# Kernel optimization log

Measured on AMD Instinct MI355X. Metric: run time of the kernel, lower is better.

## Reference

```python
import jax, jax.numpy as jnp
import numpy as np

VIS_DIM, TXT_DIM, HID = 2048, 1024, 1024


def setup_inputs() -> dict:
    key = jax.random.key(0)
    ks = jax.random.split(key, 8)
    def lin(kw, kb, fan_in, fan_out):
        bound = 1.0 / np.sqrt(fan_in)
        W = jax.random.uniform(kw, (fan_out, fan_in), jnp.float32, -bound, bound)
        b = jax.random.uniform(kb, (fan_out,), jnp.float32, -bound, bound)
        return W, b
    Wv, bv = lin(ks[0], ks[1], VIS_DIM, HID)
    Wt, bt = lin(ks[2], ks[3], TXT_DIM, HID)
    Wa, ba = lin(ks[4], ks[5], HID, 1)
    return {
        "visual_features": jax.random.normal(ks[6], (128, 256, VIS_DIM), jnp.float32),
        "text_features": jax.random.normal(ks[7], (128, TXT_DIM), jnp.float32),
        "Wv": Wv, "bv": bv, "Wt": Wt, "bt": bt, "Wa": Wa, "ba": ba,
    }


def reference(visual_features, text_features, Wv, bv, Wt, bt, Wa, ba):
    # v: (B, R, H); t: (B, 1, H) broadcast over regions
    v = jnp.einsum("brd,hd->brh", visual_features, Wv) + bv
    t = (text_features @ Wt.T + bt)[:, None, :]
    combined = jnp.tanh(v + t)                       # (B, R, H)
    scores = jnp.einsum("brh,h->br", combined, Wa[0]) + ba[0]  # (B, R)
    attention_weights = jax.nn.softmax(scores, axis=1)
    attended = jnp.einsum("br,brd->bd", attention_weights, visual_features)
    return attended, attention_weights
```

## Files before the change

kernel.cpp:

```cpp
#include <hip/hip_runtime.h>
#include <hip/hip_bf16.h>

#define VIS_DIM 2048
#define TXT_DIM 1024
#define HID     1024
#define NB      128
#define NR      256
#define M_TOT   (NB*NR)

typedef __attribute__((ext_vector_type(4))) float  f32x4;
typedef __attribute__((ext_vector_type(8))) short  short8;
typedef __attribute__((ext_vector_type(4))) unsigned short u16x4;

static __device__ __forceinline__ unsigned short f2bf(float f) {
    union { __hip_bfloat16 h; unsigned short u; } c;
    c.h = __float2bfloat16(f);
    return c.u;
}

static __device__ __forceinline__ float tanh_fast(float x) {
    float xc = fminf(fmaxf(x, -15.f), 15.f);
    float e  = __expf(2.f * xc);
    return (e - 1.f) / (e + 1.f);
}

__global__ void init_ws(float* __restrict__ scores, float* __restrict__ tbuf,
                        const float* __restrict__ bt) {
    int i = blockIdx.x * 256 + threadIdx.x;
    if (i < M_TOT) scores[i] = 0.f;
    tbuf[i] = bt[i & (HID - 1)];
}

__global__ __launch_bounds__(256) void gemm_text(const float* __restrict__ text,
                                                 const float* __restrict__ Wt,
                                                 float* __restrict__ tbuf) {
    __shared__ float As[128][33];
    __shared__ float Bs[32][33];
    const int n0  = blockIdx.x * 32;
    const int k0  = blockIdx.y * 256;
    const int tid = threadIdx.x;
    const int tm  = tid >> 3;
    const int tn  = tid & 7;
    float acc[4][4] = {};
    for (int kt = 0; kt < 8; ++kt) {
        const int k = k0 + kt * 32;
        {
            int row = tid >> 1, off = (tid & 1) * 16;
            const float* src = text + row * TXT_DIM + k + off;
            #pragma unroll
            for (int j = 0; j < 4; ++j) {
                f32x4 v = *(const f32x4*)(src + j * 4);
                As[row][off + j*4 + 0] = v.x; As[row][off + j*4 + 1] = v.y;
                As[row][off + j*4 + 2] = v.z; As[row][off + j*4 + 3] = v.w;
            }
        }
        {
            int row = tid >> 3, off = (tid & 7) * 4;
            f32x4 v = *(const f32x4*)(Wt + (size_t)(n0 + row) * TXT_DIM + k + off);
            Bs[row][off + 0] = v.x; Bs[row][off + 1] = v.y;
            Bs[row][off + 2] = v.z; Bs[row][off + 3] = v.w;
        }
        __syncthreads();
        #pragma unroll
        for (int kk = 0; kk < 32; ++kk) {
            float a[4], b[4];
            #pragma unroll
            for (int i = 0; i < 4; ++i) a[i] = As[tm*4 + i][kk];
            #pragma unroll
            for (int j = 0; j < 4; ++j) b[j] = Bs[tn*4 + j][kk];
            #pragma unroll
            for (int i = 0; i < 4; ++i)
                #pragma unroll
                for (int j = 0; j < 4; ++j) acc[i][j] += a[i] * b[j];
        }
        __syncthreads();
    }
    #pragma unroll
    for (int i = 0; i < 4; ++i)
        #pragma unroll
        for (int j = 0; j < 4; ++j)
            atomicAdd(&tbuf[(tm*4 + i) * HID + n0 + tn*4 + j], acc[i][j]);
}

#define BK 32
#define NT (VIS_DIM / BK)

static __device__ __forceinline__ int tile_off(int row, int kElem) {
    return row * 64 + (((kElem >> 3) ^ ((row >> 1) & 3)) << 4);
}

__global__ __launch_bounds__(256, 2) void gemm_vis(
        const float* __restrict__ A,
        const float* __restrict__ Bv,
        const float* __restrict__ bv,
        const float* __restrict__ wa,
        const float* __restrict__ tbuf,
        float* __restrict__ scores) {
    __shared__ __align__(16) char lds[32768];

    const int wg   = blockIdx.x;
    const int xcd  = wg & 7;
    const int loc  = wg >> 3;
    const int mb   = xcd * 32 + (loc >> 3);
    const int nb   = loc & 7;
    const int brow = mb * 128;
    const int bcol = nb * 128;

    const int tid  = threadIdx.x;
    const int lane = tid & 63;
    const int wid  = tid >> 6;
    const int wr   = wid >> 1, wc = wid & 1;

    const int srow = tid >> 3;
    const int sfs  = tid & 7;
    unsigned va0 = ((unsigned)(brow + srow      ) * VIS_DIM + sfs * 4) * 4u;
    unsigned va1 = va0 + 32u * VIS_DIM * 4u;
    unsigned va2 = va0 + 64u * VIS_DIM * 4u;
    unsigned va3 = va0 + 96u * VIS_DIM * 4u;
    unsigned vb0 = ((unsigned)(bcol + srow      ) * VIS_DIM + sfs * 4) * 4u;
    unsigned vb1 = vb0 + 32u * VIS_DIM * 4u;
    unsigned vb2 = vb0 + 64u * VIS_DIM * 4u;
    unsigned vb3 = vb0 + 96u * VIS_DIM * 4u;

    int wbyte[4];
    #pragma unroll
    for (int r = 0; r < 4; ++r) {
        int row = srow + 32 * r;
        wbyte[r] = row * 64 + (((sfs >> 1) ^ ((row >> 1) & 3)) << 4) + (sfs & 1) * 8;
    }

    f32x4 sA0, sA1, sA2, sA3, sB0, sB1, sB2, sB3;
    f32x4 tA0, tA1, tA2, tA3, tB0, tB1, tB2, tB3;
    f32x4 acc[4][4] = {};

#define GLOAD_SET(dA0,dA1,dA2,dA3,dB0,dB1,dB2,dB3)                             \
    do {                                                                       \
        asm volatile("global_load_dwordx4 %0, %1, %2"                          \
                     : "=&v"(dA0) : "v"(va0), "s"(A) : "memory");              \
        asm volatile("global_load_dwordx4 %0, %1, %2"                          \
                     : "=&v"(dA1) : "v"(va1), "s"(A) : "memory");              \
        asm volatile("global_load_dwordx4 %0, %1, %2"                          \
                     : "=&v"(dA2) : "v"(va2), "s"(A) : "memory");              \
        asm volatile("global_load_dwordx4 %0, %1, %2"                          \
                     : "=&v"(dA3) : "v"(va3), "s"(A) : "memory");              \
        asm volatile("global_load_dwordx4 %0, %1, %2"                          \
                     : "=&v"(dB0) : "v"(vb0), "s"(Bv) : "memory");             \
        asm volatile("global_load_dwordx4 %0, %1, %2"                          \
                     : "=&v"(dB1) : "v"(vb1), "s"(Bv) : "memory");             \
        asm volatile("global_load_dwordx4 %0, %1, %2"                          \
                     : "=&v"(dB2) : "v"(vb2), "s"(Bv) : "memory");             \
        asm volatile("global_load_dwordx4 %0, %1, %2"                          \
                     : "=&v"(dB3) : "v"(vb3), "s"(Bv) : "memory");             \
        va0 += BK * 4; va1 += BK * 4; va2 += BK * 4; va3 += BK * 4;            \
        vb0 += BK * 4; vb1 += BK * 4; vb2 += BK * 4; vb3 += BK * 4;            \
    } while (0)

#define GLOAD_S() GLOAD_SET(sA0,sA1,sA2,sA3,sB0,sB1,sB2,sB3)
#define GLOAD_T() GLOAD_SET(tA0,tA1,tA2,tA3,tB0,tB1,tB2,tB3)

#define VWAIT(N)                                                               \
    do {                                                                       \
        __builtin_amdgcn_sched_barrier(0);                                     \
        asm volatile("s_waitcnt vmcnt(" #N ")" ::: "memory");                  \
        __builtin_amdgcn_sched_barrier(0);                                     \
    } while (0)

#define CVT8(dst, v0)                                                          \
    do {                                                                       \
        u16x4 t_;                                                              \
        t_.x = f2bf((v0).x); t_.y = f2bf((v0).y);                              \
        t_.z = f2bf((v0).z); t_.w = f2bf((v0).w);                              \
        dst = t_;                                                              \
    } while (0)

#define LWRITE_SET(bufbase, dA0,dA1,dA2,dA3,dB0,dB1,dB2,dB3)                   \
    do {                                                                       \
        u16x4 w_;                                                              \
        char* la = lds + (bufbase);                                            \
        char* lb = lds + (bufbase) + 8192;                                     \
        CVT8(w_, dA0); *(u16x4*)(la + wbyte[0]) = w_;                          \
        CVT8(w_, dA1); *(u16x4*)(la + wbyte[1]) = w_;                          \
        CVT8(w_, dA2); *(u16x4*)(la + wbyte[2]) = w_;                          \
        CVT8(w_, dA3); *(u16x4*)(la + wbyte[3]) = w_;                          \
        CVT8(w_, dB0); *(u16x4*)(lb + wbyte[0]) = w_;                          \
        CVT8(w_, dB1); *(u16x4*)(lb + wbyte[1]) = w_;                          \
        CVT8(w_, dB2); *(u16x4*)(lb + wbyte[2]) = w_;                          \
        CVT8(w_, dB3); *(u16x4*)(lb + wbyte[3]) = w_;                          \
    } while (0)

#define LWRITE_S(bufbase) LWRITE_SET(bufbase, sA0,sA1,sA2,sA3,sB0,sB1,sB2,sB3)
#define LWRITE_T(bufbase) LWRITE_SET(bufbase, tA0,tA1,tA2,tA3,tB0,tB1,tB2,tB3)

#define COMPUTE(bufbase)                                                       \
    do {                                                                       \
        short8 af[4], bf[4];                                                   \
        const int kk = (lane >> 4) * 8;                                        \
        const char* la = lds + (bufbase);                                      \
        const char* lb = lds + (bufbase) + 8192;                               \
        _Pragma("unroll")                                                      \
        for (int m = 0; m < 4; ++m)                                            \
            af[m] = *(const short8*)(la + tile_off(wr*64 + m*16 + (lane&15), kk)); \
        _Pragma("unroll")                                                      \
        for (int n = 0; n < 4; ++n)                                            \
            bf[n] = *(const short8*)(lb + tile_off(wc*64 + n*16 + (lane&15), kk)); \
        _Pragma("unroll")                                                      \
        for (int m = 0; m < 4; ++m)                                            \
            _Pragma("unroll")                                                  \
            for (int n = 0; n < 4; ++n)                                        \
                acc[m][n] = __builtin_amdgcn_mfma_f32_16x16x32_bf16(           \
                    af[m], bf[n], acc[m][n], 0, 0, 0);                         \
    } while (0)

    GLOAD_S();
    GLOAD_T();
    VWAIT(8);
    LWRITE_S(0);
    __syncthreads();

    #pragma unroll 1
    for (int kt = 0; kt < NT - 2; kt += 2) {
        GLOAD_S();
        COMPUTE(0);
        VWAIT(8);
        LWRITE_T(16384);
        __syncthreads();
        GLOAD_T();
        COMPUTE(16384);
        VWAIT(8);
        LWRITE_S(0);
        __syncthreads();
    }
    COMPUTE(0);
    VWAIT(0);
    LWRITE_T(16384);
    __syncthreads();
    COMPUTE(16384);
#undef GLOAD_SET
#undef GLOAD_S
#undef GLOAD_T
#undef VWAIT
#undef CVT8
#undef LWRITE_SET
#undef LWRITE_S
#undef LWRITE_T
#undef COMPUTE

    const int b = brow >> 8;
    float wa_c[4], bvt_c[4];
    #pragma unroll
    for (int n = 0; n < 4; ++n) {
        int col = bcol + wc * 64 + n * 16 + (lane & 15);
        wa_c[n]  = wa[col];
        bvt_c[n] = bv[col] + tbuf[b * HID + col];
    }
    #pragma unroll
    for (int m = 0; m < 4; ++m) {
        float p0 = 0.f, p1 = 0.f, p2 = 0.f, p3 = 0.f;
        #pragma unroll
        for (int n = 0; n < 4; ++n) {
            f32x4 v = acc[m][n];
            p0 += wa_c[n] * tanh_fast(v.x + bvt_c[n]);
            p1 += wa_c[n] * tanh_fast(v.y + bvt_c[n]);
            p2 += wa_c[n] * tanh_fast(v.z + bvt_c[n]);
            p3 += wa_c[n] * tanh_fast(v.w + bvt_c[n]);
        }
        #pragma unroll
        for (int d = 1; d < 16; d <<= 1) {
            p0 += __shfl_xor(p0, d); p1 += __shfl_xor(p1, d);
            p2 += __shfl_xor(p2, d); p3 += __shfl_xor(p3, d);
        }
        if ((lane & 15) == 0) {
            int rowg = brow + wr * 64 + m * 16 + (lane >> 4) * 4;
            atomicAdd(&scores[rowg + 0], p0);
            atomicAdd(&scores[rowg + 1], p1);
            atomicAdd(&scores[rowg + 2], p2);
            atomicAdd(&scores[rowg + 3], p3);
        }
    }
}

__global__ __launch_bounds__(256) void attend(const float* __restrict__ visual,
                                              const float* __restrict__ scores,
                                              float* __restrict__ out) {
    const int chunk = blockIdx.x;
    const int b     = blockIdx.y;
    const int tid   = threadIdx.x;
    const int lane  = tid & 63;
    const int wv    = tid >> 6;

    __shared__ float wsm[NR];
    __shared__ float red[4];
    __shared__ f32x4 part[4][64];

    float s = scores[b * NR + tid];
    float mx = s;
    #pragma unroll
    for (int d = 1; d < 64; d <<= 1) mx = fmaxf(mx, __shfl_xor(mx, d));
    if (lane == 0) red[wv] = mx;
    __syncthreads();
    mx = fmaxf(fmaxf(red[0], red[1]), fmaxf(red[2], red[3]));
    float e = __expf(s - mx);
    float sum = e;
    #pragma unroll
    for (int d = 1; d < 64; d <<= 1) sum += __shfl_xor(sum, d);
    __syncthreads();
    if (lane == 0) red[wv] = sum;
    __syncthreads();
    sum = red[0] + red[1] + red[2] + red[3];
    float w = e * (1.f / sum);
    wsm[tid] = w;
    if (chunk == 0) out[(size_t)NB * VIS_DIM + b * NR + tid] = w;
    __syncthreads();

    const float* vb = visual + ((size_t)b * NR + wv * 64) * VIS_DIM + chunk * 256 + lane * 4;
    f32x4 acc = {0.f, 0.f, 0.f, 0.f};
    #pragma unroll
    for (int r = 0; r < 64; r += 4) {
        f32x4 v0 = *(const f32x4*)(vb + (size_t)(r + 0) * VIS_DIM);
        f32x4 v1 = *(const f32x4*)(vb + (size_t)(r + 1) * VIS_DIM);
        f32x4 v2 = *(const f32x4*)(vb + (size_t)(r + 2) * VIS_DIM);
        f32x4 v3 = *(const f32x4*)(vb + (size_t)(r + 3) * VIS_DIM);
        acc += wsm[wv * 64 + r + 0] * v0;
        acc += wsm[wv * 64 + r + 1] * v1;
        acc += wsm[wv * 64 + r + 2] * v2;
        acc += wsm[wv * 64 + r + 3] * v3;
    }
    part[wv][lane] = acc;
    __syncthreads();
    if (wv == 0) {
        f32x4 a = part[0][lane] + part[1][lane] + part[2][lane] + part[3][lane];
        *(f32x4*)(out + (size_t)b * VIS_DIM + chunk * 256 + lane * 4) = a;
    }
}

extern "C" void kernel_launch(void* const* d_in, const int* in_sizes, int n_in,
                              void* d_out, int out_size, void* d_ws, size_t ws_size,
                              hipStream_t stream) {
    (void)in_sizes; (void)n_in; (void)out_size; (void)ws_size;
    const float* visual = (const float*)d_in[0];
    const float* text   = (const float*)d_in[1];
    const float* Wv     = (const float*)d_in[2];
    const float* bv     = (const float*)d_in[3];
    const float* Wt     = (const float*)d_in[4];
    const float* bt     = (const float*)d_in[5];
    const float* Wa     = (const float*)d_in[6];

    float* out    = (float*)d_out;
    float* scores = (float*)d_ws;
    float* tbuf   = scores + M_TOT;

    init_ws  <<<512, 256, 0, stream>>>(scores, tbuf, bt);
    gemm_text<<<dim3(32, 4), 256, 0, stream>>>(text, Wt, tbuf);
    gemm_vis <<<2048, 256, 0, stream>>>(visual, Wv, bv, Wa, tbuf, scores);
    attend   <<<dim3(8, NB), 256, 0, stream>>>(visual, scores, out);
}
```

Measured before the change: 282.3 us.

## Deepen global-load prefetch to three register stages in GEMM main loop

Adds a third register set so global loads for the GEMM are issued two K-tiles ahead instead of one, with the waits relaxed to vmcnt(16). The aim is to hide more global memory latency behind MFMA compute. In exchange it holds 32 more VGPRs of prefetched data, which may cut occupancy. The main loop is unrolled by six tiles, so the prologue and epilogue tile counts must line up with NT.

```diff
diff --git a/kernel.cpp b/kernel.cpp
--- a/kernel.cpp
+++ b/kernel.cpp
@@ -129,8 +129,9 @@
         wbyte[r] = row * 64 + (((sfs >> 1) ^ ((row >> 1) & 3)) << 4) + (sfs & 1) * 8;
     }
 
-    f32x4 sA0, sA1, sA2, sA3, sB0, sB1, sB2, sB3;
-    f32x4 tA0, tA1, tA2, tA3, tB0, tB1, tB2, tB3;
+    f32x4 xA0, xA1, xA2, xA3, xB0, xB1, xB2, xB3;
+    f32x4 yA0, yA1, yA2, yA3, yB0, yB1, yB2, yB3;
+    f32x4 zA0, zA1, zA2, zA3, zB0, zB1, zB2, zB3;
     f32x4 acc[4][4] = {};
 
 #define GLOAD_SET(dA0,dA1,dA2,dA3,dB0,dB1,dB2,dB3)                             \
@@ -155,8 +156,9 @@
         vb0 += BK * 4; vb1 += BK * 4; vb2 += BK * 4; vb3 += BK * 4;            \
     } while (0)
 
-#define GLOAD_S() GLOAD_SET(sA0,sA1,sA2,sA3,sB0,sB1,sB2,sB3)
-#define GLOAD_T() GLOAD_SET(tA0,tA1,tA2,tA3,tB0,tB1,tB2,tB3)
+#define GLOAD_0() GLOAD_SET(xA0,xA1,xA2,xA3,xB0,xB1,xB2,xB3)
+#define GLOAD_1() GLOAD_SET(yA0,yA1,yA2,yA3,yB0,yB1,yB2,yB3)
+#define GLOAD_2() GLOAD_SET(zA0,zA1,zA2,zA3,zB0,zB1,zB2,zB3)
 
 #define VWAIT(N)                                                               \
     do {                                                                       \
@@ -188,8 +190,9 @@
         CVT8(w_, dB3); *(u16x4*)(lb + wbyte[3]) = w_;                          \
     } while (0)
 
-#define LWRITE_S(bufbase) LWRITE_SET(bufbase, sA0,sA1,sA2,sA3,sB0,sB1,sB2,sB3)
-#define LWRITE_T(bufbase) LWRITE_SET(bufbase, tA0,tA1,tA2,tA3,tB0,tB1,tB2,tB3)
+#define LWRITE_0(b) LWRITE_SET(b, xA0,xA1,xA2,xA3,xB0,xB1,xB2,xB3)
+#define LWRITE_1(b) LWRITE_SET(b, yA0,yA1,yA2,yA3,yB0,yB1,yB2,yB3)
+#define LWRITE_2(b) LWRITE_SET(b, zA0,zA1,zA2,zA3,zB0,zB1,zB2,zB3)
 
 #define COMPUTE(bufbase)                                                       \
     do {                                                                       \
@@ -211,38 +214,40 @@
                     af[m], bf[n], acc[m][n], 0, 0, 0);                         \
     } while (0)
 
-    GLOAD_S();
-    GLOAD_T();
+    GLOAD_0();
+    GLOAD_1();
     VWAIT(8);
-    LWRITE_S(0);
+    LWRITE_0(0);
+    GLOAD_2();
     __syncthreads();
 
     #pragma unroll 1
-    for (int kt = 0; kt < NT - 2; kt += 2) {
-        GLOAD_S();
-        COMPUTE(0);
-        VWAIT(8);
-        LWRITE_T(16384);
-        __syncthreads();
-        GLOAD_T();
-        COMPUTE(16384);
-        VWAIT(8);
-        LWRITE_S(0);
-        __syncthreads();
-    }
+    for (int t = 0; t < NT - 4; t += 6) {
+        GLOAD_0(); COMPUTE(0);     VWAIT(16); LWRITE_1(16384); __syncthreads();
+        GLOAD_1(); COMPUTE(16384); VWAIT(16); LWRITE_2(0);     __syncthreads();
+        GLOAD_2(); COMPUTE(0);     VWAIT(16); LWRITE_0(16384); __syncthreads();
+        GLOAD_0(); COMPUTE(16384); VWAIT(16); LWRITE_1(0);     __syncthreads();
+        GLOAD_1(); COMPUTE(0);     VWAIT(16); LWRITE_2(16384); __syncthreads();
+        GLOAD_2(); COMPUTE(16384); VWAIT(16); LWRITE_0(0);     __syncthreads();
+    }
+    GLOAD_0();
     COMPUTE(0);
-    VWAIT(0);
-    LWRITE_T(16384);
-    __syncthreads();
+    VWAIT(16); LWRITE_1(16384); __syncthreads();
+    COMPUTE(16384);
+    VWAIT(8);  LWRITE_2(0);     __syncthreads();
+    COMPUTE(0);
+    VWAIT(0);  LWRITE_0(16384); __syncthreads();
     COMPUTE(16384);
 #undef GLOAD_SET
-#undef GLOAD_S
-#undef GLOAD_T
+#undef GLOAD_0
+#undef GLOAD_1
+#undef GLOAD_2
 #undef VWAIT
 #undef CVT8
 #undef LWRITE_SET
-#undef LWRITE_S
-#undef LWRITE_T
+#undef LWRITE_0
+#undef LWRITE_1
+#undef LWRITE_2
 #undef COMPUTE
 
     const int b = brow >> 8;
```

New measurement: 286.1 us. No clear change (+1.4%).
